# Kernel optimization log

Measured on AMD Instinct MI355X. Metric: run time of the kernel, lower is better.

## Reference

```python
import jax, jax.numpy as jnp
import numpy as np

N = 131072; B = 4; PER = N // B
M = 32768; MPER = M // B; K = 16; E = M * K
NF = 16; C = 32
BNC = float(1.0 / np.sqrt(1.0 + 1e-5))  # BatchNorm1d in eval mode, default running stats (mean=0,var=1,affine=identity)
_kd = np.array([[1.,1.,1.],[-1.,1.,1.],[1.,-1.,1.],[1.,1.,-1.],[-1.,-1.,1.],[-1.,1.,-1.],[1.,-1.,-1.],[-1.,-1.,-1.]], np.float32) / np.float32(np.sqrt(3.0))
KDIRS = jnp.asarray(_kd)  # [8,3] LightKernel directions


def _ln(x, g, b):
    m = x.mean(-1, keepdims=True)
    v = ((x - m) ** 2).mean(-1, keepdims=True)
    return (x - m) / jnp.sqrt(v + 1e-5) * g + b


def _mlp2(x, w1, b1, w2, b2):
    # Seq(Lin, BN, SiLU) x2 ; BN in eval mode == multiply by BNC
    h = jax.nn.silu(BNC * (x @ w1 + b1))
    return jax.nn.silu(BNC * (h @ w2 + b2))


def setup_inputs():
    rng = np.random.default_rng(0)
    f32 = np.float32
    w = lambda fi, fo: jnp.asarray((rng.standard_normal((fi, fo)) * 0.05).astype(f32))
    dg = lambda n: jnp.asarray((rng.standard_normal(n) * 0.05).astype(f32))
    z = lambda n: jnp.zeros((n,), jnp.float32)
    o = lambda n: jnp.ones((n,), jnp.float32)
    pos = jnp.asarray((rng.standard_normal((N, 3)) * 5.0).astype(f32))
    reflectance = jnp.asarray(rng.random(N).astype(f32))
    batch = jnp.asarray(np.repeat(np.arange(B), PER).astype(np.int64))
    sf = jnp.full((B,), 10.0, jnp.float32)
    # voxel-sampled centers: MPER per cloud, within each cloud's index range
    idx = np.concatenate([b * PER + rng.choice(PER, MPER, replace=False) for b in range(B)])
    tb = np.repeat(np.arange(B), MPER)
    # radius-graph edges: K in-batch source neighbors per sampled target
    col = (rng.integers(0, PER, size=(M, K)) + tb[:, None] * PER).reshape(-1)
    row = np.repeat(np.arange(M), K)
    inp = dict(pos=pos, reflectance=reflectance, sf=sf,
               batch=batch, idx=jnp.asarray(idx.astype(np.int64)),
               col=jnp.asarray(col.astype(np.int64)), row=jnp.asarray(row.astype(np.int64)))
    inp.update(stem_ln_g=o(97), stem_ln_b=z(97), stem_w1=w(97, 64), stem_b1=z(64),
               stem_w2=w(64, C), stem_b2=z(C),
               lk_w=w(8, 3), lk_b=z(3), lk_ln_g=o(3), lk_ln_b=z(3),
               loc_w1=w(C + 7, 64), loc_b1=z(64), loc_w2=w(64, 4 * C), loc_b2=z(4 * C),
               exp_w=w(128, 512), exp_b=z(512),
               dw1_w=dg(512), dw1_b=z(512), pw1_w=w(512, 512), pw1_b=z(512),
               dw2_w=dg(512), dw2_b=z(512), pw2_w=w(512, 512), pw2_b=z(512),
               proj_w=w(512, 128), proj_b=z(128))
    return inp


def _forward(pos, reflectance, sf, batch, idx, col, row,
             stem_ln_g, stem_ln_b, stem_w1, stem_b1, stem_w2, stem_b2,
             lk_w, lk_b, lk_ln_g, lk_ln_b,
             loc_w1, loc_b1, loc_w2, loc_b2,
             exp_w, exp_b, dw1_w, dw1_b, pw1_w, pw1_b,
             dw2_w, dw2_b, pw2_w, pw2_b, proj_w, proj_b):
    # --- StemModule: positional encoding + LayerNorm(97) + MLP[97,64,32] ---
    npos = pos / sf[batch][:, None]
    cnt = jax.ops.segment_sum(jnp.ones((N,), jnp.float32), batch, num_segments=B)
    centers = jax.ops.segment_sum(npos, batch, num_segments=B) / jnp.maximum(cnt, 1.0)[:, None]
    npos = npos - centers[batch]
    freqs = 1.0 / (10000.0 ** (2.0 * jnp.arange(NF, dtype=jnp.float32) / NF))
    pe = npos[:, :, None] * freqs                                   # [N,3,NF]
    pe = jnp.concatenate([jnp.sin(pe), jnp.cos(pe)], axis=-1).reshape(N, -1)  # [N,96]
    xin = _ln(jnp.concatenate([pe, reflectance[:, None]], axis=1), stem_ln_g, stem_ln_b)
    x = _mlp2(xin, stem_w1, stem_b1, stem_w2, stem_b2)              # [N,C]
    # --- SAModule: PointNetConv on precomputed radius graph ---
    pos4 = jnp.concatenate([pos, reflectance[:, None]], axis=1)     # [N,4]
    rel = pos4[col] - pos4[idx][row]                                # [E,4] pos_j - pos_i
    rel3 = rel[:, :3]
    dirs = rel3 / (jnp.linalg.norm(rel3, axis=1, keepdims=True) + 1e-8)
    kr = dirs @ KDIRS.T                                             # [E,8] kernel responses
    ecnt = jax.ops.segment_sum(jnp.ones((E,), jnp.float32), row, num_segments=M)
    nb = jax.ops.segment_sum(kr, row, num_segments=M) / jnp.maximum(ecnt, 1.0)[:, None]  # scatter_mean
    sfeat = _ln(nb @ lk_w + lk_b, lk_ln_g, lk_ln_b)                 # [M,3]
    msg = jnp.concatenate([x[col], rel, sfeat[row]], axis=1)        # [E,C+7]
    h = _mlp2(msg, loc_w1, loc_b1, loc_w2, loc_b2)                  # [E,4C] local_nn
    agg = jax.ops.segment_max(h, row, num_segments=M)               # max aggregation [M,4C]
    # --- InvertedResidualBlock (all kernel-size-1 convs => linear / per-channel) ---
    r = agg
    o = jax.nn.silu(BNC * (agg @ exp_w + exp_b))        # expand 128->512
    o = jax.nn.silu(BNC * (o * dw1_w + dw1_b))          # depthwise conv k=1
    o = jax.nn.silu(BNC * (o @ pw1_w + pw1_b))          # pointwise conv
    o = jax.nn.silu(BNC * o)                            # BN+SiLU between DWSep blocks
    o = jax.nn.silu(BNC * (o * dw2_w + dw2_b))
    o = jax.nn.silu(BNC * (o @ pw2_w + pw2_b))
    o = BNC * o                                         # trailing BN (no act)
    o = BNC * (o @ proj_w + proj_b)                     # project 512->128 + BN
    return jax.nn.silu(o + r)                           # [M,4C]


def reference(pos, reflectance, sf, batch, idx, col, row,
              stem_ln_g, stem_ln_b, stem_w1, stem_b1, stem_w2, stem_b2,
              lk_w, lk_b, lk_ln_g, lk_ln_b,
              loc_w1, loc_b1, loc_w2, loc_b2,
              exp_w, exp_b, dw1_w, dw1_b, pw1_w, pw1_b,
              dw2_w, dw2_b, pw2_w, pw2_b, proj_w, proj_b):
    return _forward(pos, reflectance, sf, batch, idx, col, row,
                    stem_ln_g, stem_ln_b, stem_w1, stem_b1, stem_w2, stem_b2,
                    lk_w, lk_b, lk_ln_g, lk_ln_b,
                    loc_w1, loc_b1, loc_w2, loc_b2,
                    exp_w, exp_b, dw1_w, dw1_b, pw1_w, pw1_b,
                    dw2_w, dw2_b, pw2_w, pw2_b, proj_w, proj_b)
```

## Files before the change

### kernel.cpp

```cpp
#include <hip/hip_runtime.h>

typedef unsigned short u16;
typedef unsigned int   u32;
typedef __attribute__((ext_vector_type(8))) u16  u16x8;
typedef __attribute__((ext_vector_type(4))) float f32x4;

#define N_PTS   131072
#define M_PTS   32768
#define BNCF    0.9999950000374997f

__device__ __forceinline__ float b2f(u16 u) {
    u32 x = ((u32)u) << 16;
    float f;
    __builtin_memcpy(&f, &x, 4);
    return f;
}
__device__ __forceinline__ u16 f2b(float f) {
    u32 x;
    __builtin_memcpy(&x, &f, 4);
    u32 r = x + 0x7fffu + ((x >> 16) & 1u);
    return (u16)(r >> 16);
}
__device__ __forceinline__ u16 f2b_hw(float f) {
    u32 r;
    asm("v_cvt_pk_bf16_f32 %0, %1, %1" : "=v"(r) : "v"(f));
    return (u16)r;
}
__device__ __forceinline__ float silu_f(float x) {
    return x * __builtin_amdgcn_rcpf(1.0f + __expf(-x));
}

__device__ __forceinline__ f32x4 mfma_bf16(u16x8 a, u16x8 b, f32x4 c) {
    asm volatile("v_mfma_f32_16x16x32_bf16 %0, %1, %2, %0"
                 : "+v"(c) : "v"(a), "v"(b));
    return c;
}
__device__ __forceinline__ void mai_guard() {
    asm volatile("s_nop 7\n\ts_nop 7\n\ts_nop 3");
}

__device__ __forceinline__ void cp_glds16(const u16* g, u16* l) {
    typedef const __attribute__((address_space(1))) u32* gp1_t;
    typedef __attribute__((address_space(3))) u32* lp3_t;
    __builtin_amdgcn_global_load_lds((gp1_t)(unsigned long long)g,
                                     (lp3_t)(unsigned long long)l, 16, 0, 0);
}

__global__ __launch_bounds__(256) void k_prep_big(const float* __restrict__ expw, u16* __restrict__ expwt,
                                                  const float* __restrict__ pw1w, u16* __restrict__ pw1t,
                                                  const float* __restrict__ pw2w, u16* __restrict__ pw2t,
                                                  const float* __restrict__ prjw, u16* __restrict__ prjt) {
    __shared__ u16 tile[64][66];
    int bid = blockIdx.x;
    const float* W; u16* O; int K, Nn, tk, tn_;
    if (bid < 16)            { W = expw; O = expwt; K = 128; Nn = 512; tk = bid >> 3; tn_ = bid & 7; }
    else if ((bid -= 16) < 64) { W = pw1w; O = pw1t; K = 512; Nn = 512; tk = bid >> 3; tn_ = bid & 7; }
    else if ((bid -= 64) < 64) { W = pw2w; O = pw2t; K = 512; Nn = 512; tk = bid >> 3; tn_ = bid & 7; }
    else { bid -= 64;          W = prjw; O = prjt; K = 512; Nn = 128; tk = bid >> 1; tn_ = bid & 1; }
    int k0 = tk * 64, n0 = tn_ * 64;
    int c = threadIdx.x & 63, r0 = threadIdx.x >> 6;
#pragma unroll
    for (int rr = 0; rr < 16; ++rr) {
        int row = r0 * 16 + rr;
        tile[row][c] = f2b(W[(long)(k0 + row) * Nn + n0 + c]);
    }
    __syncthreads();
#pragma unroll
    for (int rr = 0; rr < 16; ++rr) {
        int row = r0 * 16 + rr;
        O[(long)(n0 + row) * K + k0 + c] = tile[c][row];
    }
}

__global__ __launch_bounds__(256) void k_prep_small(const float* __restrict__ lw1,  u16* __restrict__ lw1t,
                                                    const float* __restrict__ lw2,  u16* __restrict__ lw2t,
                                                    const float* __restrict__ sw1,  u16* __restrict__ sw1t,
                                                    const float* __restrict__ sw2,  u16* __restrict__ sw2t) {
    int idx = blockIdx.x * 256 + threadIdx.x;
    const float* W; u16* O; int K, ksh, Nn;
    if (idx < 4096)                  { W = lw1; O = lw1t; K = 39; ksh = 6; Nn = 64;  }
    else if ((idx -= 4096) < 8192)   { W = lw2; O = lw2t; K = 64; ksh = 6; Nn = 128; }
    else if ((idx -= 8192) < 8192)   { W = sw1; O = sw1t; K = 97; ksh = 7; Nn = 64;  }
    else if ((idx -= 8192) < 2048)   { W = sw2; O = sw2t; K = 64; ksh = 6; Nn = 32;  }
    else return;
    int n = idx >> ksh, k = idx & ((1 << ksh) - 1);
    O[idx] = (k < K) ? f2b(W[(long)k * Nn + n]) : (u16)0;
}

__global__ __launch_bounds__(256) void k_centers(const float* __restrict__ pos,
                                                 const float* __restrict__ sfv,
                                                 const int* __restrict__ batch,
                                                 float* __restrict__ acc) {
    __shared__ float ls[16];
    int t = threadIdx.x, lane = t & 63, wave = t >> 6;
    int i = blockIdx.x * 256 + t;
    int b = batch[blockIdx.x * 256];
    float inv = 1.0f / sfv[b];
    float x = pos[i * 3 + 0] * inv;
    float y = pos[i * 3 + 1] * inv;
    float z = pos[i * 3 + 2] * inv;
#pragma unroll
    for (int m = 1; m < 64; m <<= 1) {
        x += __shfl_xor(x, m);
        y += __shfl_xor(y, m);
        z += __shfl_xor(z, m);
    }
    if (lane == 0) { ls[wave * 4 + 0] = x; ls[wave * 4 + 1] = y; ls[wave * 4 + 2] = z; }
    __syncthreads();
    if (t < 3) {
        float s = ls[t] + ls[4 + t] + ls[8 + t] + ls[12 + t];
        atomicAdd(&acc[b * 4 + t], s);
    }
    if (t == 3) atomicAdd(&acc[b * 4 + 3], 256.0f);
}

__global__ __launch_bounds__(256, 3) void k_stem(const float* __restrict__ pos,
                                              const float* __restrict__ refl,
                                              const float* __restrict__ sfv,
                                              const int* __restrict__ batch,
                                              const float* __restrict__ cacc,
                                              const float* __restrict__ g,
                                              const float* __restrict__ bb,
                                              const u16* __restrict__ w1t,
                                              const float* __restrict__ b1,
                                              const u16* __restrict__ w2t,
                                              const float* __restrict__ b2,
                                              u16* __restrict__ xout) {
    __shared__ u16 xs[128][136];
    __shared__ u16 hb[128][72];
    const float FLO[8] = {
        1.0f, 0.31622776601683794f, 0.1f, 0.031622776601683791f,
        0.01f, 0.0031622776601683794f, 0.001f, 0.00031622776601683794f};
    const float FHI[8] = {
        0.0001f, 3.1622776601683795e-05f, 1e-05f, 3.1622776601683796e-06f,
        1e-06f, 3.1622776601683797e-07f, 1e-07f, 3.1622776601683792e-08f};
    int t = threadIdx.x;
    int wave = t >> 6, lane = t & 63;
    int quad = lane >> 4, l16 = lane & 15;
    int mt0 = wave * 2;

    {
        int p = t >> 1, half = t & 1;
        int i = blockIdx.x * 128 + p;
        int b = batch[i];
        float s = 1.0f / sfv[b];
        float cnt = fmaxf(cacc[b * 4 + 3], 1.0f);
        float npv[3];
#pragma unroll
        for (int d = 0; d < 3; ++d)
            npv[d] = pos[i * 3 + d] * s - cacc[b * 4 + d] / cnt;

        float fq[8];
#pragma unroll
        for (int f = 0; f < 8; ++f) fq[f] = half ? FHI[f] : FLO[f];

        float sv[3][8], cv[3][8];
        float sum = 0.0f, sq = 0.0f;
#pragma unroll
        for (int d = 0; d < 3; ++d) {
#pragma unroll
            for (int f = 0; f < 8; ++f) {
                float a = npv[d] * fq[f];
                float s_, c_;
                __sincosf(a, &s_, &c_);
                sv[d][f] = s_;
                cv[d][f] = c_;
                sum += s_ + c_;
                sq += s_ * s_ + c_ * c_;
            }
        }
        float rf = refl[i];
        if (half == 0) { sum += rf; sq += rf * rf; }
        sum += __shfl_xor(sum, 1);
        sq  += __shfl_xor(sq, 1);

        float m = sum * (1.0f / 97.0f);
        float var = sq * (1.0f / 97.0f) - m * m;
        float rstd = rsqrtf(fmaxf(var, 0.0f) + 1e-5f);

#pragma unroll
        for (int d = 0; d < 3; ++d) {
            int c0 = d * 32 + half * 8;
            {
                f32x4 g0  = *(const f32x4*)(g + c0);
                f32x4 g1  = *(const f32x4*)(g + c0 + 4);
                f32x4 bb0 = *(const f32x4*)(bb + c0);
                f32x4 bb1 = *(const f32x4*)(bb + c0 + 4);
                u16 tmp[8];
#pragma unroll
                for (int f = 0; f < 4; ++f) {
                    tmp[f]     = f2b_hw((sv[d][f]     - m) * rstd * g0[f] + bb0[f]);
                    tmp[4 + f] = f2b_hw((sv[d][4 + f] - m) * rstd * g1[f] + bb1[f]);
                }
                *(uint4*)(&xs[p][c0]) = *(uint4*)tmp;
            }
            int c1 = d * 32 + 16 + half * 8;
            {
                f32x4 g0  = *(const f32x4*)(g + c1);
                f32x4 g1  = *(const f32x4*)(g + c1 + 4);
                f32x4 bb0 = *(const f32x4*)(bb + c1);
                f32x4 bb1 = *(const f32x4*)(bb + c1 + 4);
                u16 tmp[8];
#pragma unroll
                for (int f = 0; f < 4; ++f) {
                    tmp[f]     = f2b_hw((cv[d][f]     - m) * rstd * g0[f] + bb0[f]);
                    tmp[4 + f] = f2b_hw((cv[d][4 + f] - m) * rstd * g1[f] + bb1[f]);
                }
                *(uint4*)(&xs[p][c1]) = *(uint4*)tmp;
            }
        }
        if (half == 0) {
            float v = rf;
            u16 tmp[8];
            tmp[0] = f2b_hw((v - m) * rstd * g[96] + bb[96]);
#pragma unroll
            for (int f = 1; f < 8; ++f) tmp[f] = 0;
            *(uint4*)(&xs[p][96]) = *(uint4*)tmp;
        } else {
            uint4 z = {0, 0, 0, 0};
            *(uint4*)(&xs[p][104]) = z;
            *(uint4*)(&xs[p][112]) = z;
            *(uint4*)(&xs[p][120]) = z;
        }
    }
    __syncthreads();

    {
        f32x4 acc[2][4];
#pragma unroll
        for (int i = 0; i < 2; ++i)
#pragma unroll
            for (int j = 0; j < 4; ++j) acc[i][j] = (f32x4){0.f, 0.f, 0.f, 0.f};
#pragma unroll
        for (int kk = 0; kk < 128; kk += 32) {
            u16x8 af[2], bfr[4];
#pragma unroll
            for (int i = 0; i < 2; ++i)
                af[i] = *(const u16x8*)(&xs[(mt0 + i) * 16 + l16][kk + quad * 8]);
#pragma unroll
            for (int j = 0; j < 4; ++j)
                bfr[j] = *(const u16x8*)(w1t + (j * 16 + l16) * 128 + kk + quad * 8);
#pragma unroll
            for (int i = 0; i < 2; ++i)
#pragma unroll
                for (int j = 0; j < 4; ++j)
                    acc[i][j] = mfma_bf16(af[i], bfr[j], acc[i][j]);
        }
        mai_guard();
#pragma unroll
        for (int i = 0; i < 2; ++i)
#pragma unroll
            for (int j = 0; j < 4; ++j) {
                f32x4 c = acc[i][j];
                int n = j * 16 + l16;
                float bn = b1[n] * BNCF;
#pragma unroll
                for (int r = 0; r < 4; ++r)
                    hb[(mt0 + i) * 16 + quad * 4 + r][n] =
                        f2b_hw(silu_f(fmaf(BNCF, c[r], bn)));
            }
    }
    __syncthreads();

    {
        f32x4 acc[2][2];
#pragma unroll
        for (int i = 0; i < 2; ++i)
#pragma unroll
            for (int j = 0; j < 2; ++j) acc[i][j] = (f32x4){0.f, 0.f, 0.f, 0.f};
#pragma unroll
        for (int kk = 0; kk < 64; kk += 32) {
            u16x8 af[2], bfr[2];
#pragma unroll
            for (int i = 0; i < 2; ++i)
                af[i] = *(const u16x8*)(&hb[(mt0 + i) * 16 + l16][kk + quad * 8]);
#pragma unroll
            for (int j = 0; j < 2; ++j)
                bfr[j] = *(const u16x8*)(w2t + (j * 16 + l16) * 64 + kk + quad * 8);
#pragma unroll
            for (int i = 0; i < 2; ++i)
#pragma unroll
                for (int j = 0; j < 2; ++j)
                    acc[i][j] = mfma_bf16(af[i], bfr[j], acc[i][j]);
        }
        mai_guard();
#pragma unroll
        for (int i = 0; i < 2; ++i)
#pragma unroll
            for (int j = 0; j < 2; ++j) {
                f32x4 c = acc[i][j];
                int n = j * 16 + l16;
                float bn = b2[n] * BNCF;
#pragma unroll
                for (int r = 0; r < 4; ++r) {
                    int m = (mt0 + i) * 16 + quad * 4 + r;
                    long ig = (long)blockIdx.x * 128 + m;
                    xout[ig * 32 + n] = f2b_hw(silu_f(fmaf(BNCF, c[r], bn)));
                }
            }
    }
}

__global__ __launch_bounds__(256, 4) void k_edge(const float* __restrict__ pos,
                                              const float* __restrict__ refl,
                                              const int* __restrict__ idxp,
                                              const int* __restrict__ colp,
                                              const u16* __restrict__ xfeat,
                                              const float* __restrict__ lkw,
                                              const float* __restrict__ lkb,
                                              const float* __restrict__ lng,
                                              const float* __restrict__ lnb,
                                              const u16* __restrict__ w1t,
                                              const float* __restrict__ b1,
                                              const u16* __restrict__ w2t,
                                              const float* __restrict__ b2,
                                              float* __restrict__ agg,
                                              u16* __restrict__ aggb,
                                              int rbase) {
    __shared__ u16 uni16[128 * 72];
    __shared__ u16 ws[128 * 72];
    __shared__ float b1s[64];
    __shared__ float b2s[128];
    int t = threadIdx.x;
    int r0 = (rbase + blockIdx.x) * 8;
    long e0 = (long)r0 * 16;
    int wave = t >> 6, lane = t & 63;
    int quad = lane >> 4, l16 = lane & 15;
    int mt0 = wave * 2;

    for (int u = t; u < 512; u += 256) {
        int row = u >> 3, c8 = (u & 7) * 8;
        *(uint4*)(&ws[row * 72 + c8]) = *(const uint4*)(w1t + row * 64 + c8);
    }
    if (t < 64) b1s[t] = b1[t] * BNCF;
    if (t < 128) b2s[t] = b2[t] * BNCF;

    for (int u = t; u < 512; u += 256) {
        int e = u >> 2, seg = u & 3;
        int c = colp[e0 + e];
        uint4 d = *(const uint4*)(xfeat + (long)c * 32 + seg * 8);
        *(uint4*)(&uni16[e * 72 + seg * 8]) = d;
    }
    if (t < 128) {
        int e = t;
        int r = r0 + (e >> 4);
        int c = colp[e0 + e];
        int ci = idxp[r];
        float dx = pos[c * 3 + 0] - pos[ci * 3 + 0];
        float dy = pos[c * 3 + 1] - pos[ci * 3 + 1];
        float dz = pos[c * 3 + 2] - pos[ci * 3 + 2];
        float dr = refl[c] - refl[ci];

        float nrm = sqrtf(dx * dx + dy * dy + dz * dz);
        float inv = __builtin_amdgcn_rcpf(nrm + 1e-8f);
        float ux = dx * inv, uy = dy * inv, uz = dz * inv;
#pragma unroll
        for (int msk = 1; msk <= 8; msk <<= 1) {
            ux += __shfl_xor(ux, msk);
            uy += __shfl_xor(uy, msk);
            uz += __shfl_xor(uz, msk);
        }
        const float S3_16 = 0.57735026918962576f * (1.0f / 16.0f);
        const float sxk[8] = {1, -1, 1, 1, -1, -1, 1, -1};
        const float syk[8] = {1, 1, -1, 1, -1, 1, -1, -1};
        const float szk[8] = {1, 1, 1, -1, 1, -1, -1, -1};
        float sc0 = lkb[0], sc1 = lkb[1], sc2 = lkb[2];
#pragma unroll
        for (int j = 0; j < 8; ++j) {
            float nb = (sxk[j] * ux + syk[j] * uy + szk[j] * uz) * S3_16;
            sc0 += nb * lkw[j * 3 + 0];
            sc1 += nb * lkw[j * 3 + 1];
            sc2 += nb * lkw[j * 3 + 2];
        }
        float mm = (sc0 + sc1 + sc2) * (1.0f / 3.0f);
        float vv = ((sc0 - mm) * (sc0 - mm) + (sc1 - mm) * (sc1 - mm) +
                    (sc2 - mm) * (sc2 - mm)) * (1.0f / 3.0f);
        float rstd = rsqrtf(fmaxf(vv, 0.0f) + 1e-5f);

        u16 tmp[8];
        tmp[0] = f2b_hw(dx);
        tmp[1] = f2b_hw(dy);
        tmp[2] = f2b_hw(dz);
        tmp[3] = f2b_hw(dr);
        tmp[4] = f2b_hw((sc0 - mm) * rstd * lng[0] + lnb[0]);
        tmp[5] = f2b_hw((sc1 - mm) * rstd * lng[1] + lnb[1]);
        tmp[6] = f2b_hw((sc2 - mm) * rstd * lng[2] + lnb[2]);
        tmp[7] = 0;
        *(uint4*)(&uni16[e * 72 + 32]) = *(uint4*)tmp;
        uint4 z = {0, 0, 0, 0};
        *(uint4*)(&uni16[e * 72 + 40]) = z;
        *(uint4*)(&uni16[e * 72 + 48]) = z;
        *(uint4*)(&uni16[e * 72 + 56]) = z;
    }
    __syncthreads();

    {
        f32x4 acc[2][4];
#pragma unroll
        for (int i = 0; i < 2; ++i)
#pragma unroll
            for (int j = 0; j < 4; ++j) acc[i][j] = (f32x4){0.f, 0.f, 0.f, 0.f};
#pragma unroll
        for (int kk = 0; kk < 64; kk += 32) {
            u16x8 af[2], bfr[4];
#pragma unroll
            for (int i = 0; i < 2; ++i)
                af[i] = *(const u16x8*)(&uni16[((mt0 + i) * 16 + l16) * 72 + kk + quad * 8]);
#pragma unroll
            for (int j = 0; j < 4; ++j)
                bfr[j] = *(const u16x8*)(&ws[(j * 16 + l16) * 72 + kk + quad * 8]);
#pragma unroll
            for (int i = 0; i < 2; ++i)
#pragma unroll
                for (int j = 0; j < 4; ++j)
                    acc[i][j] = mfma_bf16(af[i], bfr[j], acc[i][j]);
        }
        mai_guard();
#pragma unroll
        for (int i = 0; i < 2; ++i)
#pragma unroll
            for (int j = 0; j < 4; ++j) {
                f32x4 c = acc[i][j];
                int n = j * 16 + l16;
#pragma unroll
                for (int r = 0; r < 4; ++r) {
                    float v = silu_f(fmaf(BNCF, c[r], b1s[n]));
                    uni16[((mt0 + i) * 16 + quad * 4 + r) * 72 + n] = f2b_hw(v);
                }
            }
    }
    __syncthreads();

    for (int u = t; u < 1024; u += 256) {
        int row = u >> 3, c8 = (u & 7) * 8;
        *(uint4*)(&ws[row * 72 + c8]) = *(const uint4*)(w2t + row * 64 + c8);
    }
    __syncthreads();

    {
        f32x4 acc[2][8];
#pragma unroll
        for (int i = 0; i < 2; ++i)
#pragma unroll
            for (int j = 0; j < 8; ++j) acc[i][j] = (f32x4){0.f, 0.f, 0.f, 0.f};
#pragma unroll
        for (int kk = 0; kk < 64; kk += 32) {
            u16x8 af[2], bfr[8];
#pragma unroll
            for (int i = 0; i < 2; ++i)
                af[i] = *(const u16x8*)(&uni16[((mt0 + i) * 16 + l16) * 72 + kk + quad * 8]);
#pragma unroll
            for (int j = 0; j < 8; ++j)
                bfr[j] = *(const u16x8*)(&ws[(j * 16 + l16) * 72 + kk + quad * 8]);
#pragma unroll
            for (int i = 0; i < 2; ++i)
#pragma unroll
                for (int j = 0; j < 8; ++j)
                    acc[i][j] = mfma_bf16(af[i], bfr[j], acc[i][j]);
        }
        mai_guard();
#pragma unroll
        for (int i = 0; i < 2; ++i) {
            int rg = r0 + mt0 + i;
#pragma unroll
            for (int j = 0; j < 8; ++j) {
                f32x4 c = acc[i][j];
                int n = j * 16 + l16;
                float mx = fmaxf(fmaxf(c[0], c[1]), fmaxf(c[2], c[3]));
                float mn = fminf(fminf(c[0], c[1]), fminf(c[2], c[3]));
                mx = fmaxf(mx, __shfl_xor(mx, 16));
                mx = fmaxf(mx, __shfl_xor(mx, 32));
                mn = fminf(mn, __shfl_xor(mn, 16));
                mn = fminf(mn, __shfl_xor(mn, 32));
                if (quad == 0) {
                    float v = fmaxf(silu_f(fmaf(BNCF, mx, b2s[n])),
                                    silu_f(fmaf(BNCF, mn, b2s[n])));
                    agg[(long)rg * 128 + n] = v;
                    aggb[(long)rg * 128 + n] = f2b_hw(v);
                }
            }
        }
    }
}

template <int EPI, int OD, int NXB, int K, int Nn>
__global__ __launch_bounds__(256, 4) void k_mgemm(const u16* __restrict__ A,
                                               const u16* __restrict__ Bt,
                                               const float* __restrict__ bias,
                                               const float* __restrict__ dww,
                                               const float* __restrict__ dwb,
                                               const float* __restrict__ res,
                                               void* __restrict__ Ov) {
    __shared__ u16 As[128 * 64];
    __shared__ u16 Bs[128 * 64];
    int t = threadIdx.x;
    int wave = t >> 6, lane = t & 63;
    int quad = lane >> 4, l16 = lane & 15;
    int bx, by;
    if (NXB == 4) {
        int d = blockIdx.x;
        int q = d >> 5, r = d & 31;
        by = q * 8 + (r & 7);
        bx = r >> 3;
    } else {
        bx = 0; by = blockIdx.x;
    }
    int R0 = by * 128, C0 = bx * 128;
    int wm = (wave & 1) * 64, wn = (wave >> 1) * 64;

    int srow = (lane >> 3);
    int sch  = lane & 7;

    f32x4 acc[4][4];
#pragma unroll
    for (int i = 0; i < 4; ++i)
#pragma unroll
        for (int j = 0; j < 4; ++j) acc[i][j] = (f32x4){0.f, 0.f, 0.f, 0.f};

    for (int k0 = 0; k0 < K; k0 += 64) {
#pragma unroll
        for (int it = 0; it < 4; ++it) {
            int base = wave * 32 + it * 8;
            int row = base + srow;
            int gch = (sch ^ (row & 7)) << 3;
            cp_glds16(A  + (long)(R0 + row) * K + k0 + gch, &As[base * 64]);
            cp_glds16(Bt + (long)(C0 + row) * K + k0 + gch, &Bs[base * 64]);
        }
        __syncthreads();
#pragma unroll
        for (int kk = 0; kk < 64; kk += 32) {
            int kb = kk >> 3;
            u16x8 af[4], bfr[4];
#pragma unroll
            for (int tm = 0; tm < 4; ++tm) {
                int r = wm + tm * 16 + l16;
                af[tm] = *(const u16x8*)(&As[r * 64 + (((kb + quad) ^ (r & 7)) << 3)]);
            }
#pragma unroll
            for (int tn = 0; tn < 4; ++tn) {
                int r = wn + tn * 16 + l16;
                bfr[tn] = *(const u16x8*)(&Bs[r * 64 + (((kb + quad) ^ (r & 7)) << 3)]);
            }
#pragma unroll
            for (int tm = 0; tm < 4; ++tm)
#pragma unroll
                for (int tn = 0; tn < 4; ++tn)
                    acc[tm][tn] = mfma_bf16(af[tm], bfr[tn], acc[tm][tn]);
        }
        __syncthreads();
    }

    float bnA[4], dnA[4], dbA[4];
#pragma unroll
    for (int tn = 0; tn < 4; ++tn) {
        int n = C0 + wn + tn * 16 + l16;
        bnA[tn] = bias[n] * BNCF;
        if (EPI == 0 || EPI == 1) { dnA[tn] = dww[n] * BNCF; dbA[tn] = dwb[n] * BNCF; }
        else { dnA[tn] = 0.0f; dbA[tn] = 0.0f; }
    }
    mai_guard();
#pragma unroll
    for (int tm = 0; tm < 4; ++tm) {
#pragma unroll
        for (int tn = 0; tn < 4; ++tn) {
            f32x4 c = acc[tm][tn];
            int n = C0 + wn + tn * 16 + l16;
#pragma unroll
            for (int r = 0; r < 4; ++r) {
                int m = R0 + wm + tm * 16 + quad * 4 + r;
                float v = c[r];
                if (EPI == 0) {
                    v = silu_f(fmaf(BNCF, v, bnA[tn]));
                    v = silu_f(fmaf(v, dnA[tn], dbA[tn]));
                } else if (EPI == 1) {
                    v = silu_f(fmaf(BNCF, v, bnA[tn]));
                    v = silu_f(BNCF * v);
                    v = silu_f(fmaf(v, dnA[tn], dbA[tn]));
                } else if (EPI == 2) {
                    v = silu_f(fmaf(BNCF, v, bnA[tn]));
                    v = BNCF * v;
                } else {
                    v = fmaf(BNCF, v, bnA[tn]);
                    v = silu_f(v + res[(long)m * 128 + n]);
                }
                if (OD == 0)
                    ((u16*)Ov)[(long)m * Nn + n] = f2b_hw(v);
                else
                    ((float*)Ov)[(long)m * Nn + n] = v;
            }
        }
    }
}

extern "C" void kernel_launch(void* const* d_in, const int* in_sizes, int n_in,
                              void* d_out, int out_size, void* d_ws, size_t ws_size,
                              hipStream_t stream) {
    const float* pos   = (const float*)d_in[0];
    const float* refl  = (const float*)d_in[1];
    const float* sfv   = (const float*)d_in[2];
    const int*   batch = (const int*)d_in[3];
    const int*   idxp  = (const int*)d_in[4];
    const int*   colp  = (const int*)d_in[5];
    const float* s_g  = (const float*)d_in[7];
    const float* s_b  = (const float*)d_in[8];
    const float* s_w1 = (const float*)d_in[9];
    const float* s_b1 = (const float*)d_in[10];
    const float* s_w2 = (const float*)d_in[11];
    const float* s_b2 = (const float*)d_in[12];
    const float* lkw  = (const float*)d_in[13];
    const float* lkb  = (const float*)d_in[14];
    const float* lng  = (const float*)d_in[15];
    const float* lnb  = (const float*)d_in[16];
    const float* l_w1 = (const float*)d_in[17];
    const float* l_b1 = (const float*)d_in[18];
    const float* l_w2 = (const float*)d_in[19];
    const float* l_b2 = (const float*)d_in[20];
    const float* expw = (const float*)d_in[21];
    const float* expb = (const float*)d_in[22];
    const float* dw1w = (const float*)d_in[23];
    const float* dw1b = (const float*)d_in[24];
    const float* pw1w = (const float*)d_in[25];
    const float* pw1b = (const float*)d_in[26];
    const float* dw2w = (const float*)d_in[27];
    const float* dw2b = (const float*)d_in[28];
    const float* pw2w = (const float*)d_in[29];
    const float* pw2b = (const float*)d_in[30];
    const float* prjw = (const float*)d_in[31];
    const float* prjb = (const float*)d_in[32];

    char* ws = (char*)d_ws;
    float* cent  = (float*)(ws + 0);
    float* agg   = (float*)(ws + 393280);
    u16*   aggb  = (u16*)(ws + 17170496);
    u16*   u1    = (u16*)(ws + 25559104);
    u16*   u2    = (u16*)(ws + 59113536);
    u16*   xf    = (u16*)(ws + 59113536);
    u16*   expwt = (u16*)(ws + 92667968);
    u16*   pw1t  = (u16*)(ws + 92799040);
    u16*   pw2t  = (u16*)(ws + 93323328);
    u16*   prjt  = (u16*)(ws + 93847616);
    u16*   lw1t  = (u16*)(ws + 93978688);
    u16*   lw2t  = (u16*)(ws + 93986880);
    u16*   sw1t  = (u16*)(ws + 94003264);
    u16*   sw2t  = (u16*)(ws + 94019648);

    k_prep_big<<<160, 256, 0, stream>>>(expw, expwt, pw1w, pw1t, pw2w, pw2t, prjw, prjt);
    k_prep_small<<<88, 256, 0, stream>>>(l_w1, lw1t, l_w2, lw2t, s_w1, sw1t, s_w2, sw2t);

    hipMemsetAsync(cent, 0, 64, stream);
    k_centers<<<512, 256, 0, stream>>>(pos, sfv, batch, cent);
    k_stem<<<1024, 256, 0, stream>>>(pos, refl, sfv, batch, cent, s_g, s_b,
                                     sw1t, s_b1, sw2t, s_b2, xf);
    k_edge<<<2048, 256, 0, stream>>>(pos, refl, idxp, colp, xf,
                                     lkw, lkb, lng, lnb,
                                     lw1t, l_b1, lw2t, l_b2, agg, aggb, 0);
    k_edge<<<2048, 256, 0, stream>>>(pos, refl, idxp, colp, xf,
                                     lkw, lkb, lng, lnb,
                                     lw1t, l_b1, lw2t, l_b2, agg, aggb, 2048);

    dim3 blk(256);
    k_mgemm<0, 0, 4, 128, 512><<<1024, blk, 0, stream>>>(aggb, expwt, expb, dw1w, dw1b,
                                                         nullptr, u1);
    k_mgemm<1, 0, 4, 512, 512><<<1024, blk, 0, stream>>>(u1, pw1t, pw1b, dw2w, dw2b,
                                                         nullptr, u2);
    k_mgemm<2, 0, 4, 512, 512><<<1024, blk, 0, stream>>>(u2, pw2t, pw2b, nullptr, nullptr,
                                                         nullptr, u1);
    k_mgemm<3, 1, 1, 512, 128><<<256, blk, 0, stream>>>(u1, prjt, prjb, nullptr, nullptr,
                                                        agg, d_out);
}
```

Measured before the change: 304.6 us.

## Merge prep kernels and edge launches, reuse stem LDS, split edge gather work

Merges the two weight-prep kernels and the center-accumulator memset into one launch, and merges the two half-size edge launches into a single 4096-block launch, cutting launch overhead. In k_stem the hidden activations now reuse the xs shared buffer instead of a separate hb array, lowering LDS use so the occupancy hint rises from 3 to 4 blocks. In k_edge the upper 128 threads do the neighbor feature gather while the lower 128 compute geometry, so the two run concurrently instead of one after the other. Reusing xs relies on a barrier between the first GEMM's reads and the hidden writes; if none exists, this is a race.

```diff
diff --git a/kernel.cpp b/kernel.cpp
--- a/kernel.cpp
+++ b/kernel.cpp
@@ -46,37 +46,40 @@
                                      (lp3_t)(unsigned long long)l, 16, 0, 0);
 }
 
-__global__ __launch_bounds__(256) void k_prep_big(const float* __restrict__ expw, u16* __restrict__ expwt,
-                                                  const float* __restrict__ pw1w, u16* __restrict__ pw1t,
-                                                  const float* __restrict__ pw2w, u16* __restrict__ pw2t,
-                                                  const float* __restrict__ prjw, u16* __restrict__ prjt) {
+__global__ __launch_bounds__(256) void k_prep(const float* __restrict__ expw, u16* __restrict__ expwt,
+                                              const float* __restrict__ pw1w, u16* __restrict__ pw1t,
+                                              const float* __restrict__ pw2w, u16* __restrict__ pw2t,
+                                              const float* __restrict__ prjw, u16* __restrict__ prjt,
+                                              const float* __restrict__ lw1,  u16* __restrict__ lw1t,
+                                              const float* __restrict__ lw2,  u16* __restrict__ lw2t,
+                                              const float* __restrict__ sw1,  u16* __restrict__ sw1t,
+                                              const float* __restrict__ sw2,  u16* __restrict__ sw2t,
+                                              float* __restrict__ cent) {
     __shared__ u16 tile[64][66];
     int bid = blockIdx.x;
-    const float* W; u16* O; int K, Nn, tk, tn_;
-    if (bid < 16)            { W = expw; O = expwt; K = 128; Nn = 512; tk = bid >> 3; tn_ = bid & 7; }
-    else if ((bid -= 16) < 64) { W = pw1w; O = pw1t; K = 512; Nn = 512; tk = bid >> 3; tn_ = bid & 7; }
-    else if ((bid -= 64) < 64) { W = pw2w; O = pw2t; K = 512; Nn = 512; tk = bid >> 3; tn_ = bid & 7; }
-    else { bid -= 64;          W = prjw; O = prjt; K = 512; Nn = 128; tk = bid >> 1; tn_ = bid & 1; }
-    int k0 = tk * 64, n0 = tn_ * 64;
-    int c = threadIdx.x & 63, r0 = threadIdx.x >> 6;
-#pragma unroll
-    for (int rr = 0; rr < 16; ++rr) {
-        int row = r0 * 16 + rr;
-        tile[row][c] = f2b(W[(long)(k0 + row) * Nn + n0 + c]);
-    }
-    __syncthreads();
-#pragma unroll
-    for (int rr = 0; rr < 16; ++rr) {
-        int row = r0 * 16 + rr;
-        O[(long)(n0 + row) * K + k0 + c] = tile[c][row];
-    }
-}
-
-__global__ __launch_bounds__(256) void k_prep_small(const float* __restrict__ lw1,  u16* __restrict__ lw1t,
-                                                    const float* __restrict__ lw2,  u16* __restrict__ lw2t,
-                                                    const float* __restrict__ sw1,  u16* __restrict__ sw1t,
-                                                    const float* __restrict__ sw2,  u16* __restrict__ sw2t) {
-    int idx = blockIdx.x * 256 + threadIdx.x;
+    if (bid < 160) {
+        const float* W; u16* O; int K, Nn, tk, tn_;
+        if (bid < 16)              { W = expw; O = expwt; K = 128; Nn = 512; tk = bid >> 3; tn_ = bid & 7; }
+        else if ((bid -= 16) < 64) { W = pw1w; O = pw1t;  K = 512; Nn = 512; tk = bid >> 3; tn_ = bid & 7; }
+        else if ((bid -= 64) < 64) { W = pw2w; O = pw2t;  K = 512; Nn = 512; tk = bid >> 3; tn_ = bid & 7; }
+        else { bid -= 64;            W = prjw; O = prjt;  K = 512; Nn = 128; tk = bid >> 1; tn_ = bid & 1; }
+        int k0 = tk * 64, n0 = tn_ * 64;
+        int c = threadIdx.x & 63, r0 = threadIdx.x >> 6;
+#pragma unroll
+        for (int rr = 0; rr < 16; ++rr) {
+            int row = r0 * 16 + rr;
+            tile[row][c] = f2b(W[(long)(k0 + row) * Nn + n0 + c]);
+        }
+        __syncthreads();
+#pragma unroll
+        for (int rr = 0; rr < 16; ++rr) {
+            int row = r0 * 16 + rr;
+            O[(long)(n0 + row) * K + k0 + c] = tile[c][row];
+        }
+        return;
+    }
+    int idx = (bid - 160) * 256 + threadIdx.x;
+    if (bid == 247 && threadIdx.x < 16) cent[threadIdx.x] = 0.0f;
     const float* W; u16* O; int K, ksh, Nn;
     if (idx < 4096)                  { W = lw1; O = lw1t; K = 39; ksh = 6; Nn = 64;  }
     else if ((idx -= 4096) < 8192)   { W = lw2; O = lw2t; K = 64; ksh = 6; Nn = 128; }
@@ -114,7 +117,7 @@
     if (t == 3) atomicAdd(&acc[b * 4 + 3], 256.0f);
 }
 
-__global__ __launch_bounds__(256, 3) void k_stem(const float* __restrict__ pos,
+__global__ __launch_bounds__(256, 4) void k_stem(const float* __restrict__ pos,
                                               const float* __restrict__ refl,
                                               const float* __restrict__ sfv,
                                               const int* __restrict__ batch,
@@ -127,7 +130,6 @@
                                               const float* __restrict__ b2,
                                               u16* __restrict__ xout) {
     __shared__ u16 xs[128][136];
-    __shared__ u16 hb[128][72];
     const float FLO[8] = {
         1.0f, 0.31622776601683794f, 0.1f, 0.031622776601683791f,
         0.01f, 0.0031622776601683794f, 0.001f, 0.00031622776601683794f};
@@ -256,7 +258,7 @@
                 float bn = b1[n] * BNCF;
 #pragma unroll
                 for (int r = 0; r < 4; ++r)
-                    hb[(mt0 + i) * 16 + quad * 4 + r][n] =
+                    xs[(mt0 + i) * 16 + quad * 4 + r][n] =
                         f2b_hw(silu_f(fmaf(BNCF, c[r], bn)));
             }
     }
@@ -273,7 +275,7 @@
             u16x8 af[2], bfr[2];
 #pragma unroll
             for (int i = 0; i < 2; ++i)
-                af[i] = *(const u16x8*)(&hb[(mt0 + i) * 16 + l16][kk + quad * 8]);
+                af[i] = *(const u16x8*)(&xs[(mt0 + i) * 16 + l16][kk + quad * 8]);
 #pragma unroll
             for (int j = 0; j < 2; ++j)
                 bfr[j] = *(const u16x8*)(w2t + (j * 16 + l16) * 64 + kk + quad * 8);
@@ -315,14 +317,13 @@
                                               const u16* __restrict__ w2t,
                                               const float* __restrict__ b2,
                                               float* __restrict__ agg,
-                                              u16* __restrict__ aggb,
-                                              int rbase) {
+                                              u16* __restrict__ aggb) {
     __shared__ u16 uni16[128 * 72];
     __shared__ u16 ws[128 * 72];
     __shared__ float b1s[64];
     __shared__ float b2s[128];
     int t = threadIdx.x;
-    int r0 = (rbase + blockIdx.x) * 8;
+    int r0 = blockIdx.x * 8;
     long e0 = (long)r0 * 16;
     int wave = t >> 6, lane = t & 63;
     int quad = lane >> 4, l16 = lane & 15;
@@ -335,13 +336,14 @@
     if (t < 64) b1s[t] = b1[t] * BNCF;
     if (t < 128) b2s[t] = b2[t] * BNCF;
 
-    for (int u = t; u < 512; u += 256) {
-        int e = u >> 2, seg = u & 3;
-        int c = colp[e0 + e];
-        uint4 d = *(const uint4*)(xfeat + (long)c * 32 + seg * 8);
-        *(uint4*)(&uni16[e * 72 + seg * 8]) = d;
-    }
-    if (t < 128) {
+    if (t >= 128) {
+        for (int u = t - 128; u < 512; u += 128) {
+            int e = u >> 2, seg = u & 3;
+            int c = colp[e0 + e];
+            uint4 d = *(const uint4*)(xfeat + (long)c * 32 + seg * 8);
+            *(uint4*)(&uni16[e * 72 + seg * 8]) = d;
+        }
+    } else {
         int e = t;
         int r = r0 + (e >> 4);
         int c = colp[e0 + e];
@@ -644,19 +646,16 @@
     u16*   sw1t  = (u16*)(ws + 94003264);
     u16*   sw2t  = (u16*)(ws + 94019648);
 
-    k_prep_big<<<160, 256, 0, stream>>>(expw, expwt, pw1w, pw1t, pw2w, pw2t, prjw, prjt);
-    k_prep_small<<<88, 256, 0, stream>>>(l_w1, lw1t, l_w2, lw2t, s_w1, sw1t, s_w2, sw2t);
-
-    hipMemsetAsync(cent, 0, 64, stream);
+    k_prep<<<248, 256, 0, stream>>>(expw, expwt, pw1w, pw1t, pw2w, pw2t, prjw, prjt,
+                                    l_w1, lw1t, l_w2, lw2t, s_w1, sw1t, s_w2, sw2t,
+                                    cent);
+
     k_centers<<<512, 256, 0, stream>>>(pos, sfv, batch, cent);
     k_stem<<<1024, 256, 0, stream>>>(pos, refl, sfv, batch, cent, s_g, s_b,
                                      sw1t, s_b1, sw2t, s_b2, xf);
-    k_edge<<<2048, 256, 0, stream>>>(pos, refl, idxp, colp, xf,
+    k_edge<<<4096, 256, 0, stream>>>(pos, refl, idxp, colp, xf,
                                      lkw, lkb, lng, lnb,
-                                     lw1t, l_b1, lw2t, l_b2, agg, aggb, 0);
-    k_edge<<<2048, 256, 0, stream>>>(pos, refl, idxp, colp, xf,
-                                     lkw, lkb, lng, lnb,
-                                     lw1t, l_b1, lw2t, l_b2, agg, aggb, 2048);
+                                     lw1t, l_b1, lw2t, l_b2, agg, aggb);
 
     dim3 blk(256);
     k_mgemm<0, 0, 4, 128, 512><<<1024, blk, 0, stream>>>(aggb, expwt, expb, dw1w, dw1b,
```

Result: faster. 294.2 us (-3.4%).
